# Kernel optimization log

Measured on AMD Instinct MI355X. Metric: run time of the kernel, lower is better.

The kernel has to match this reference:

```python
import jax, jax.numpy as jnp
import numpy as np

B, T, V, E, H = 32, 512, 20000, 300, 512


def setup_inputs() -> dict:
    key = jax.random.key(0)
    k1, k2, k3, k4 = jax.random.split(key, 4)
    tokens = jax.random.randint(k1, (B, T), 0, V, dtype=jnp.int32)
    emb = jax.random.normal(k2, (V, E), dtype=jnp.float32)
    # Keras LSTM: kernel [E, 4H], recurrent_kernel [H, 4H], bias [4H]
    W = jax.random.normal(k3, (E, 4 * H), dtype=jnp.float32) * (1.0 / np.sqrt(E))
    U = jax.random.normal(k4, (H, 4 * H), dtype=jnp.float32) * (1.0 / np.sqrt(H))
    b = jnp.zeros((4 * H,), dtype=jnp.float32)
    return {"tokens": tokens, "emb": emb, "W": W, "U": U, "b": b}


def _lstm_last_state(x, W, U, b):
    # x: [B, T, E].  Gate order (Keras): i, f, g(candidate), o.
    h0 = jnp.zeros((x.shape[0], H), dtype=x.dtype)
    c0 = jnp.zeros((x.shape[0], H), dtype=x.dtype)
    # Precompute input projections for all timesteps: [T, B, 4H]
    xz = jnp.einsum('bte,eg->tbg', x, W) + b

    def step(carry, xz_t):
        h, c = carry
        z = xz_t + h @ U                      # [B, 4H]
        i, f, g, o = jnp.split(z, 4, axis=-1)
        i = jax.nn.sigmoid(i)
        f = jax.nn.sigmoid(f)
        g = jnp.tanh(g)
        o = jax.nn.sigmoid(o)
        c = f * c + i * g
        h = o * jnp.tanh(c)
        return (h, c), None

    (h, c), _ = jax.lax.scan(step, (h0, c0), xz)
    return h, c


def reference(tokens, emb, W, U, b):
    x = emb[tokens]                            # [B, T, E] embedding lookup
    hidden, cell = _lstm_last_state(x, W, U, b)
    return (hidden, cell)                      # Encoder returns (hidden, cell)
```

## Files before the change

kernel.cpp:

```cpp
#include <hip/hip_runtime.h>
#include <hip/hip_bf16.h>

typedef unsigned short u16;
typedef unsigned int u32;
typedef unsigned long long u64;
typedef short  s16x8 __attribute__((ext_vector_type(8)));
typedef float  f32x4 __attribute__((ext_vector_type(4)));
typedef u32    u32x4 __attribute__((ext_vector_type(4)));

#define T_STEPS 512
#define BATCH   32
#define HID     512
#define EMBD    300
#define NGATE   2048

#define XZ_OFF   0ull
#define XZ_BYTES (512ull*32*2048*4)
#define UB_OFF   (XZ_OFF + XZ_BYTES)
#define UB_BYTES (2048ull*512*2)
#define WT_OFF   (UB_OFF + UB_BYTES)
#define WT_BYTES (2048ull*320*2)
#define HB_OFF   (WT_OFF + WT_BYTES)
#define HB_BYTES (2ull*8192*4)

__device__ inline u16 f2b(float f) {
  u32 u = __builtin_bit_cast(u32, f);
  return (u16)((u + 0x7fffu + ((u >> 16) & 1u)) >> 16);
}

__device__ inline void st64_agent(u64* p, u64 v) {
  __hip_atomic_store(p, v, __ATOMIC_RELAXED, __HIP_MEMORY_SCOPE_AGENT);
}

__global__ __launch_bounds__(64) void pack_w(const float* __restrict__ W, u16* __restrict__ wt) {
  int n = blockIdx.x;
  for (int i = 0; i < 5; ++i) {
    int k = i * 64 + threadIdx.x;
    float v = (k < EMBD) ? W[(size_t)k * NGATE + n] : 0.f;
    u32 off = ((u32)(2 * k)) ^ (((u32)(n & 7)) << 4);
    *(u16*)((char*)wt + (size_t)n * 640 + off) = f2b(v);
  }
}

__global__ __launch_bounds__(64) void pack_u(const float* __restrict__ U, u16* __restrict__ ub) {
  int blk = blockIdx.x;
  int w = blk >> 6, nl = blk & 63;
  int gcol = (nl & 3) * 512 + w * 16 + (nl >> 2);
  for (int i = 0; i < 8; ++i) {
    int k = i * 64 + threadIdx.x;
    float v = U[(size_t)k * NGATE + gcol];
    *(u16*)((char*)ub + (size_t)blk * 1024 + 2 * k) = f2b(v);
  }
}

__global__ __launch_bounds__(256) void xz_gemm(const int* __restrict__ tokens,
                                               const float* __restrict__ emb,
                                               const u16* __restrict__ wt,
                                               const float* __restrict__ bias,
                                               float* __restrict__ xz) {
  extern __shared__ char smem[];
  const int tid = threadIdx.x;
  const int lane = tid & 63, wv = tid >> 6;
  const int m0 = (blockIdx.x >> 5) * 64;
  const int n0 = (blockIdx.x & 31) * 64;

  {
    int row = tid >> 2, q = tid & 3;
    int tok = tokens[m0 + row];
    const float* er = emb + (size_t)tok * EMBD;
    for (int i = 0; i < 10; ++i) {
      int k = q * 80 + i * 8;
      float4 lo = {0, 0, 0, 0}, hi = {0, 0, 0, 0};
      if (k <= 296) lo = *(const float4*)(er + k);
      if (k <= 292) hi = *(const float4*)(er + k + 4);
      u16 u[8] = {f2b(lo.x), f2b(lo.y), f2b(lo.z), f2b(lo.w),
                  f2b(hi.x), f2b(hi.y), f2b(hi.z), f2b(hi.w)};
      int kc = q * 10 + i;
      *(uint4*)(smem + kc * 1040 + row * 16) = *(uint4*)u;
    }
  }
  {
    const uint4* src = (const uint4*)((const char*)wt + (size_t)n0 * 640);
    for (int i = 0; i < 10; ++i)
      *(uint4*)(smem + 41600 + (i * 256 + tid) * 16) = src[i * 256 + tid];
  }
  __syncthreads();

  const int mq = wv >> 1, nq = wv & 1;
  const int arow = lane & 15, kq4 = lane >> 4;
  f32x4 acc[2][2] = {};
#pragma unroll
  for (int ks = 0; ks < 10; ++ks) {
    s16x8 af[2], bfr[2];
#pragma unroll
    for (int mt = 0; mt < 2; ++mt) {
      int row = mq * 32 + mt * 16 + arow;
      int kc = ks * 4 + kq4;
      af[mt] = *(const s16x8*)(smem + kc * 1040 + row * 16);
    }
#pragma unroll
    for (int nt = 0; nt < 2; ++nt) {
      int nl = nq * 32 + nt * 16 + arow;
      u32 kb = (u32)(ks * 64 + (kq4 << 4));
      bfr[nt] = *(const s16x8*)(smem + 41600 + nl * 640 + (kb ^ (((u32)(nl & 7)) << 4)));
    }
#pragma unroll
    for (int mt = 0; mt < 2; ++mt)
#pragma unroll
      for (int nt = 0; nt < 2; ++nt)
        acc[mt][nt] = __builtin_amdgcn_mfma_f32_16x16x32_bf16(af[mt], bfr[nt], acc[mt][nt], 0, 0, 0);
  }
#pragma unroll
  for (int mt = 0; mt < 2; ++mt)
#pragma unroll
    for (int nt = 0; nt < 2; ++nt) {
      int gn = n0 + nq * 32 + nt * 16 + arow;
      float bv = bias[gn];
      int g = gn >> 9, j = gn & 511;
      size_t inner = (size_t)((j >> 4) * 64 + g * 16 + (j & 15));
#pragma unroll
      for (int r = 0; r < 4; ++r) {
        int gm = m0 + mq * 32 + mt * 16 + (kq4 << 2) + r;
        int tt = gm & 511, bb = gm >> 9;
        xz[(size_t)(tt * 32 + bb) * 2048 + inner] = acc[mt][nt][r] + bv;
      }
    }
}

__global__ __launch_bounds__(256) void lstm_persist(const float* __restrict__ xz,
                                                    const u16* __restrict__ ub,
                                                    u32* __restrict__ hbuf,
                                                    float* __restrict__ out) {
  extern __shared__ char smem[];
  char* hl = smem;
  const int tid = threadIdx.x;
  const int lane = tid & 63, wv = tid >> 6;
  const int wg = blockIdx.x;

  const int arow = lane & 15, kq = lane >> 4;
  const int nl = wv * 16 + arow;
  const u32 aswz = ((u32)(arow & 7)) << 4;
  const int j0 = wg * 16;
  const int jl = 4 * wv + kq;
  float c0 = 0.f, c1 = 0.f;

  s16x8 ureg[16];
  {
    const char* up = (const char*)ub + (size_t)(wg * 64 + nl) * 1024 + (kq << 4);
#pragma unroll
    for (int ks = 0; ks < 16; ++ks) ureg[ks] = *(const s16x8*)(up + ks * 64);
  }

  const u32 vo0 = (u32)(tid * 16 + 1 * 4096), vo1 = (u32)(tid * 16 + 3 * 4096);
  const u32 vo2 = (u32)(tid * 16 + 5 * 4096), vo3 = (u32)(tid * 16 + 7 * 4096);
  const u32 hrow0 = (u32)(tid >> 6);
  const u32 hcolb = (u32)((tid & 63) * 16);

  const int pb   = (kq & 1) ? (arow + 16) : arow;
  const u32 pidx64 = (u32)(pb * 128 + wg * 4 + wv);

  float xzv[2][4];
  {
    const float* p = xz + (size_t)arow * 2048 + wg * 64 + jl;
#pragma unroll
    for (int g = 0; g < 4; ++g) {
      xzv[0][g] = p[g * 16];
      xzv[1][g] = p[16 * 2048 + g * 16];
    }
  }
  __syncthreads();

  for (int t = 0; t < T_STEPS; ++t) {
    if (t > 0) {
      u32 tg = (((u32)t >> 1) + 1u) & 3u;
      u32 pat = (tg & 1u) | ((tg >> 1) << 16);
      const u64 sb = (u64)(uintptr_t)hbuf + (u64)((t & 1) * 32768);
      u32x4 q0, q1, q2, q3, q4, q5, q6, q7;
      int tries = 0;
      for (;;) {
        asm volatile(
          "global_load_dwordx4 %0, %8, %12 offset:-4096 sc0 sc1\n\t"
          "global_load_dwordx4 %1, %8, %12 sc0 sc1\n\t"
          "global_load_dwordx4 %2, %9, %12 offset:-4096 sc0 sc1\n\t"
          "global_load_dwordx4 %3, %9, %12 sc0 sc1\n\t"
          "global_load_dwordx4 %4, %10, %12 offset:-4096 sc0 sc1\n\t"
          "global_load_dwordx4 %5, %10, %12 sc0 sc1\n\t"
          "global_load_dwordx4 %6, %11, %12 offset:-4096 sc0 sc1\n\t"
          "global_load_dwordx4 %7, %11, %12 sc0 sc1\n\t"
          "s_waitcnt vmcnt(0)"
          : "=&v"(q0), "=&v"(q1), "=&v"(q2), "=&v"(q3),
            "=&v"(q4), "=&v"(q5), "=&v"(q6), "=&v"(q7)
          : "v"(vo0), "v"(vo1), "v"(vo2), "v"(vo3), "s"(sb)
          : "memory");
        u32 x0 = (q0.x ^ pat) | (q0.y ^ pat) | (q0.z ^ pat) | (q0.w ^ pat);
        u32 x1 = (q1.x ^ pat) | (q1.y ^ pat) | (q1.z ^ pat) | (q1.w ^ pat);
        u32 x2 = (q2.x ^ pat) | (q2.y ^ pat) | (q2.z ^ pat) | (q2.w ^ pat);
        u32 x3 = (q3.x ^ pat) | (q3.y ^ pat) | (q3.z ^ pat) | (q3.w ^ pat);
        u32 x4 = (q4.x ^ pat) | (q4.y ^ pat) | (q4.z ^ pat) | (q4.w ^ pat);
        u32 x5 = (q5.x ^ pat) | (q5.y ^ pat) | (q5.z ^ pat) | (q5.w ^ pat);
        u32 x6 = (q6.x ^ pat) | (q6.y ^ pat) | (q6.z ^ pat) | (q6.w ^ pat);
        u32 x7 = (q7.x ^ pat) | (q7.y ^ pat) | (q7.z ^ pat) | (q7.w ^ pat);
        u32 bad = (x0 | x1 | x2 | x3 | x4 | x5 | x6 | x7) & 0x00010001u;
        if (bad == 0 || ++tries > 65536) break;
        __builtin_amdgcn_s_sleep(1);
      }
#define HW(L, Q) { u32 r_ = hrow0 + 4u * (L);                                  \
        u32 off_ = r_ * 1024u + (hcolb ^ ((r_ & 7u) << 4));                    \
        *(u32x4*)(hl + off_) = (Q); }
      HW(0, q0) HW(1, q1) HW(2, q2) HW(3, q3)
      HW(4, q4) HW(5, q5) HW(6, q6) HW(7, q7)
#undef HW
    }
    __syncthreads();

    f32x4 acc0 = {0, 0, 0, 0}, acc1 = {0, 0, 0, 0};
    if (t > 0) {
#pragma unroll
      for (int ks = 0; ks < 16; ++ks) {
        u32 kb = (u32)(ks * 64 + (kq << 4));
        s16x8 h0 = *(const s16x8*)(hl + arow * 1024 + (kb ^ aswz));
        s16x8 h1 = *(const s16x8*)(hl + (arow + 16) * 1024 + (kb ^ aswz));
        acc0 = __builtin_amdgcn_mfma_f32_16x16x32_bf16(ureg[ks], h0, acc0, 0, 0, 0);
        acc1 = __builtin_amdgcn_mfma_f32_16x16x32_bf16(ureg[ks], h1, acc1, 0, 0, 0);
      }
    }

    float hov[2], cov[2];
#pragma unroll
    for (int e = 0; e < 2; ++e) {
      f32x4 zr = e ? acc1 : acc0;
      float zi = zr[0] + xzv[e][0];
      float zf = zr[1] + xzv[e][1];
      float zg = zr[2] + xzv[e][2];
      float zo = zr[3] + xzv[e][3];
      float ig = 1.f / (1.f + __expf(-zi));
      float fg = 1.f / (1.f + __expf(-zf));
      float gg = 1.f - 2.f / (__expf(2.f * zg) + 1.f);
      float og = 1.f / (1.f + __expf(-zo));
      float cc = e ? c1 : c0;
      cc = fg * cc + ig * gg;
      float hh = og * (1.f - 2.f / (__expf(2.f * cc) + 1.f));
      if (e) c1 = cc; else c0 = cc;
      hov[e] = hh; cov[e] = cc;
    }

    if (t < T_STEPS - 1) {
      u32 pk = (u32)f2b(hov[0]) | ((u32)f2b(hov[1]) << 16);
      u32 pr = (u32)__shfl_xor((int)pk, 16, 64);
      u32 val = (kq & 1) ? ((pr >> 16) | (pk & 0xFFFF0000u))
                         : ((pk & 0xFFFFu) | (pr << 16));
      u32 tg2 = (((u32)(t + 1) >> 1) + 1u) & 3u;
      val = (val & 0xFFFEFFFEu) | (tg2 & 1u) | ((tg2 >> 1) << 16);
      u32 v2 = (u32)__shfl_xor((int)val, 32, 64);
      if (kq < 2) {
        u64 wide = (u64)val | ((u64)v2 << 32);
        st64_agent((u64*)(hbuf + (size_t)((t + 1) & 1) * 8192) + pidx64, wide);
      }
      {
        const float* p = xz + ((size_t)(t + 1) * 32 + arow) * 2048 + wg * 64 + jl;
#pragma unroll
        for (int g = 0; g < 4; ++g) {
          xzv[0][g] = p[g * 16];
          xzv[1][g] = p[16 * 2048 + g * 16];
        }
      }
    } else {
      int j = j0 + jl;
      out[arow * 512 + j]                 = hov[0];
      out[(arow + 16) * 512 + j]          = hov[1];
      out[16384 + arow * 512 + j]         = cov[0];
      out[16384 + (arow + 16) * 512 + j]  = cov[1];
    }
  }
}

extern "C" void kernel_launch(void* const* d_in, const int* in_sizes, int n_in,
                              void* d_out, int out_size, void* d_ws, size_t ws_size,
                              hipStream_t stream) {
  const int*   tokens = (const int*)d_in[0];
  const float* emb    = (const float*)d_in[1];
  const float* W      = (const float*)d_in[2];
  const float* U      = (const float*)d_in[3];
  const float* bias   = (const float*)d_in[4];
  float* out = (float*)d_out;
  char*  ws  = (char*)d_ws;

  float* xz   = (float*)(ws + XZ_OFF);
  u16*   ub   = (u16*)(ws + UB_OFF);
  u16*   wt   = (u16*)(ws + WT_OFF);
  u32*   hbuf = (u32*)(ws + HB_OFF);

  hipMemsetAsync(hbuf, 0, HB_BYTES, stream);
  pack_w<<<2048, 64, 0, stream>>>(W, wt);
  pack_u<<<2048, 64, 0, stream>>>(U, ub);
  xz_gemm<<<8192, 256, 82560, stream>>>(tokens, emb, wt, bias, xz);
  lstm_persist<<<32, 256, 32768, stream>>>(xz, ub, hbuf, out);
}
```

Baseline: 1.762 ms.

## Fuse input-projection GEMM and LSTM recurrence into one kernel with per-timestep counters

Merges the xz GEMM and the persistent LSTM kernel into a single launch. The first 32 blocks run the recurrence while the remaining blocks compute input projections in time order, two timesteps per M-tile. Each GEMM block bumps a per-tile counter that the recurrence blocks poll before reading xz. The intent is to overlap the projection GEMM with the serial recurrence and remove a launch boundary. This relies on the 32 persistent blocks being co-resident with the GEMM blocks, and the spin-wait gives up after a bounded number of tries, which could read stale data.

```diff
diff --git a/kernel.cpp b/kernel.cpp
--- a/kernel.cpp
+++ b/kernel.cpp
@@ -22,14 +22,32 @@
 #define WT_BYTES (2048ull*320*2)
 #define HB_OFF   (WT_OFF + WT_BYTES)
 #define HB_BYTES (2ull*8192*4)
+#define CNT_OFF  (HB_OFF + HB_BYTES)
+#define CNT_BYTES 1024ull
 
 __device__ inline u16 f2b(float f) {
   u32 u = __builtin_bit_cast(u32, f);
   return (u16)((u + 0x7fffu + ((u >> 16) & 1u)) >> 16);
 }
 
+__device__ inline void st32_agent(u32* p, u32 v) {
+  __hip_atomic_store(p, v, __ATOMIC_RELAXED, __HIP_MEMORY_SCOPE_AGENT);
+}
 __device__ inline void st64_agent(u64* p, u64 v) {
   __hip_atomic_store(p, v, __ATOMIC_RELAXED, __HIP_MEMORY_SCOPE_AGENT);
+}
+__device__ inline u32 ld32_agent(const u32* p) {
+  return __hip_atomic_load(p, __ATOMIC_RELAXED, __HIP_MEMORY_SCOPE_AGENT);
+}
+__device__ inline float ldxz(const float* p) {
+  return __builtin_bit_cast(float, ld32_agent((const u32*)p));
+}
+__device__ inline void wait_pair(const u32* c) {
+  int tries = 0;
+  while (ld32_agent(c) < 32u) {
+    if (++tries > (1 << 22)) break;
+    __builtin_amdgcn_s_sleep(2);
+  }
 }
 
 __global__ __launch_bounds__(64) void pack_w(const float* __restrict__ W, u16* __restrict__ wt) {
@@ -53,89 +71,98 @@
   }
 }
 
-__global__ __launch_bounds__(256) void xz_gemm(const int* __restrict__ tokens,
-                                               const float* __restrict__ emb,
-                                               const u16* __restrict__ wt,
-                                               const float* __restrict__ bias,
-                                               float* __restrict__ xz) {
+__global__ __launch_bounds__(256) void fused_enc(const int* __restrict__ tokens,
+                                                 const float* __restrict__ emb,
+                                                 const u16* __restrict__ wt,
+                                                 const float* __restrict__ bias,
+                                                 const u16* __restrict__ ub,
+                                                 float* __restrict__ xz,
+                                                 u32* __restrict__ hbuf,
+                                                 u32* __restrict__ cnt,
+                                                 float* __restrict__ out) {
   extern __shared__ char smem[];
   const int tid = threadIdx.x;
+  const int bid = blockIdx.x;
   const int lane = tid & 63, wv = tid >> 6;
-  const int m0 = (blockIdx.x >> 5) * 64;
-  const int n0 = (blockIdx.x & 31) * 64;
-
-  {
-    int row = tid >> 2, q = tid & 3;
-    int tok = tokens[m0 + row];
-    const float* er = emb + (size_t)tok * EMBD;
-    for (int i = 0; i < 10; ++i) {
-      int k = q * 80 + i * 8;
-      float4 lo = {0, 0, 0, 0}, hi = {0, 0, 0, 0};
-      if (k <= 296) lo = *(const float4*)(er + k);
-      if (k <= 292) hi = *(const float4*)(er + k + 4);
-      u16 u[8] = {f2b(lo.x), f2b(lo.y), f2b(lo.z), f2b(lo.w),
-                  f2b(hi.x), f2b(hi.y), f2b(hi.z), f2b(hi.w)};
-      int kc = q * 10 + i;
-      *(uint4*)(smem + kc * 1040 + row * 16) = *(uint4*)u;
-    }
-  }
-  {
-    const uint4* src = (const uint4*)((const char*)wt + (size_t)n0 * 640);
-    for (int i = 0; i < 10; ++i)
-      *(uint4*)(smem + 41600 + (i * 256 + tid) * 16) = src[i * 256 + tid];
-  }
-  __syncthreads();
-
-  const int mq = wv >> 1, nq = wv & 1;
-  const int arow = lane & 15, kq4 = lane >> 4;
-  f32x4 acc[2][2] = {};
-#pragma unroll
-  for (int ks = 0; ks < 10; ++ks) {
-    s16x8 af[2], bfr[2];
-#pragma unroll
-    for (int mt = 0; mt < 2; ++mt) {
-      int row = mq * 32 + mt * 16 + arow;
-      int kc = ks * 4 + kq4;
-      af[mt] = *(const s16x8*)(smem + kc * 1040 + row * 16);
-    }
-#pragma unroll
-    for (int nt = 0; nt < 2; ++nt) {
-      int nl = nq * 32 + nt * 16 + arow;
-      u32 kb = (u32)(ks * 64 + (kq4 << 4));
-      bfr[nt] = *(const s16x8*)(smem + 41600 + nl * 640 + (kb ^ (((u32)(nl & 7)) << 4)));
+
+  if (bid >= 32) {
+    const int gbid = bid - 32;
+    const int mtile = gbid >> 5;
+    const int n0 = (gbid & 31) * 64;
+    const int t0 = mtile * 2;
+
+    {
+      int row = tid >> 2, q = tid & 3;
+      int tok = tokens[(row & 31) * 512 + t0 + (row >> 5)];
+      const float* er = emb + (size_t)tok * EMBD;
+      for (int i = 0; i < 10; ++i) {
+        int k = q * 80 + i * 8;
+        float4 lo = {0, 0, 0, 0}, hi = {0, 0, 0, 0};
+        if (k <= 296) lo = *(const float4*)(er + k);
+        if (k <= 292) hi = *(const float4*)(er + k + 4);
+        u16 u[8] = {f2b(lo.x), f2b(lo.y), f2b(lo.z), f2b(lo.w),
+                    f2b(hi.x), f2b(hi.y), f2b(hi.z), f2b(hi.w)};
+        int kc = q * 10 + i;
+        *(uint4*)(smem + kc * 1040 + row * 16) = *(uint4*)u;
+      }
+    }
+    {
+      const uint4* src = (const uint4*)((const char*)wt + (size_t)n0 * 640);
+      for (int i = 0; i < 10; ++i)
+        *(uint4*)(smem + 41600 + (i * 256 + tid) * 16) = src[i * 256 + tid];
+    }
+    __syncthreads();
+
+    const int mq = wv >> 1, nq = wv & 1;
+    const int arow = lane & 15, kq4 = lane >> 4;
+    f32x4 acc[2][2] = {};
+#pragma unroll
+    for (int ks = 0; ks < 10; ++ks) {
+      s16x8 af[2], bfr[2];
+#pragma unroll
+      for (int mt = 0; mt < 2; ++mt) {
+        int row = mq * 32 + mt * 16 + arow;
+        int kc = ks * 4 + kq4;
+        af[mt] = *(const s16x8*)(smem + kc * 1040 + row * 16);
+      }
+#pragma unroll
+      for (int nt = 0; nt < 2; ++nt) {
+        int nl = nq * 32 + nt * 16 + arow;
+        u32 kb = (u32)(ks * 64 + (kq4 << 4));
+        bfr[nt] = *(const s16x8*)(smem + 41600 + nl * 640 + (kb ^ (((u32)(nl & 7)) << 4)));
+      }
+#pragma unroll
+      for (int mt = 0; mt < 2; ++mt)
+#pragma unroll
+        for (int nt = 0; nt < 2; ++nt)
+          acc[mt][nt] = __builtin_amdgcn_mfma_f32_16x16x32_bf16(af[mt], bfr[nt], acc[mt][nt], 0, 0, 0);
     }
 #pragma unroll
     for (int mt = 0; mt < 2; ++mt)
 #pragma unroll
-      for (int nt = 0; nt < 2; ++nt)
-        acc[mt][nt] = __builtin_amdgcn_mfma_f32_16x16x32_bf16(af[mt], bfr[nt], acc[mt][nt], 0, 0, 0);
-  }
-#pragma unroll
-  for (int mt = 0; mt < 2; ++mt)
-#pragma unroll
-    for (int nt = 0; nt < 2; ++nt) {
-      int gn = n0 + nq * 32 + nt * 16 + arow;
-      float bv = bias[gn];
-      int g = gn >> 9, j = gn & 511;
-      size_t inner = (size_t)((j >> 4) * 64 + g * 16 + (j & 15));
-#pragma unroll
-      for (int r = 0; r < 4; ++r) {
-        int gm = m0 + mq * 32 + mt * 16 + (kq4 << 2) + r;
-        int tt = gm & 511, bb = gm >> 9;
-        xz[(size_t)(tt * 32 + bb) * 2048 + inner] = acc[mt][nt][r] + bv;
-      }
-    }
-}
-
-__global__ __launch_bounds__(256) void lstm_persist(const float* __restrict__ xz,
-                                                    const u16* __restrict__ ub,
-                                                    u32* __restrict__ hbuf,
-                                                    float* __restrict__ out) {
-  extern __shared__ char smem[];
+      for (int nt = 0; nt < 2; ++nt) {
+        int gn = n0 + nq * 32 + nt * 16 + arow;
+        float bv = bias[gn];
+        int g = gn >> 9, j = gn & 511;
+        size_t inner = (size_t)((j >> 4) * 64 + g * 16 + (j & 15));
+#pragma unroll
+        for (int r = 0; r < 4; ++r) {
+          int lr = mq * 32 + mt * 16 + (kq4 << 2) + r;
+          int tt = t0 + (lr >> 5), bb = lr & 31;
+          float v = acc[mt][nt][r] + bv;
+          st32_agent((u32*)xz + (size_t)(tt * 32 + bb) * 2048 + inner,
+                     __builtin_bit_cast(u32, v));
+        }
+      }
+    asm volatile("s_waitcnt vmcnt(0)" ::: "memory");
+    __syncthreads();
+    if (tid == 0)
+      __hip_atomic_fetch_add(&cnt[mtile], 1u, __ATOMIC_RELAXED, __HIP_MEMORY_SCOPE_AGENT);
+    return;
+  }
+
   char* hl = smem;
-  const int tid = threadIdx.x;
-  const int lane = tid & 63, wv = tid >> 6;
-  const int wg = blockIdx.x;
+  const int wg = bid;
 
   const int arow = lane & 15, kq = lane >> 4;
   const int nl = wv * 16 + arow;
@@ -161,11 +188,12 @@
 
   float xzv[2][4];
   {
+    wait_pair(&cnt[0]);
     const float* p = xz + (size_t)arow * 2048 + wg * 64 + jl;
 #pragma unroll
     for (int g = 0; g < 4; ++g) {
-      xzv[0][g] = p[g * 16];
-      xzv[1][g] = p[16 * 2048 + g * 16];
+      xzv[0][g] = ldxz(p + g * 16);
+      xzv[1][g] = ldxz(p + 16 * 2048 + g * 16);
     }
   }
   __syncthreads();
@@ -257,11 +285,12 @@
         st64_agent((u64*)(hbuf + (size_t)((t + 1) & 1) * 8192) + pidx64, wide);
       }
       {
+        if (((t + 1) & 1) == 0) wait_pair(&cnt[(t + 1) >> 1]);
         const float* p = xz + ((size_t)(t + 1) * 32 + arow) * 2048 + wg * 64 + jl;
 #pragma unroll
         for (int g = 0; g < 4; ++g) {
-          xzv[0][g] = p[g * 16];
-          xzv[1][g] = p[16 * 2048 + g * 16];
+          xzv[0][g] = ldxz(p + g * 16);
+          xzv[1][g] = ldxz(p + 16 * 2048 + g * 16);
         }
       }
     } else {
@@ -289,10 +318,11 @@
   u16*   ub   = (u16*)(ws + UB_OFF);
   u16*   wt   = (u16*)(ws + WT_OFF);
   u32*   hbuf = (u32*)(ws + HB_OFF);
-
-  hipMemsetAsync(hbuf, 0, HB_BYTES, stream);
+  u32*   cnt  = (u32*)(ws + CNT_OFF);
+
+  hipMemsetAsync(ws + HB_OFF, 0, HB_BYTES + CNT_BYTES, stream);
   pack_w<<<2048, 64, 0, stream>>>(W, wt);
   pack_u<<<2048, 64, 0, stream>>>(U, ub);
-  xz_gemm<<<8192, 256, 82560, stream>>>(tokens, emb, wt, bias, xz);
-  lstm_persist<<<32, 256, 32768, stream>>>(xz, ub, hbuf, out);
-}
+  fused_enc<<<32 + 8192, 256, 82560, stream>>>(tokens, emb, wt, bias, ub,
+                                               xz, hbuf, cnt, out);
+}
```

Result: faster. 1.596 ms (median of 2 runs) (-9.5%).
